# Kernel tuning notes

Measured on AMD Instinct MI355X. Metric: run time of the kernel, lower is better.

Reference implementation:

```python
import jax, jax.numpy as jnp
import numpy as np
import math

FMAPS = [(80, 0.06), (40, 0.12), (20, 0.24), (10, 0.48), (5, 0.72)]
SPLITS = [0, 6400, 8000, 8400, 8500, 8525]
N_LEVELS = 5
N_CAND = 9
ALPHA_REG = 1.0   # config.reg_weights
GAMMA, F_ALPHA = 2.0, 0.25


def _make_priors():
    ps = []
    for f, s in FMAPS:
        c = (np.arange(f, dtype=np.float32) + 0.5) / f
        cy, cx = np.meshgrid(c, c, indexing="ij")
        ps.append(np.stack([cx.ravel(), cy.ravel(),
                            np.full(f * f, s, np.float32),
                            np.full(f * f, s, np.float32)], 1))
    return jnp.asarray(np.concatenate(ps, 0))


def cxcy_to_xy(b):
    return jnp.concatenate([b[..., :2] - b[..., 2:] / 2, b[..., :2] + b[..., 2:] / 2], -1)


def xy_to_cxcy(b):
    return jnp.concatenate([(b[..., :2] + b[..., 2:]) / 2, b[..., 2:] - b[..., :2]], -1)


def gcxgcy_to_cxcy(g, priors):
    cxcy = g[..., :2] * priors[..., 2:] / 10.0 + priors[..., :2]
    wh = jnp.exp(g[..., 2:] / 5.0) * priors[..., 2:]
    return jnp.concatenate([cxcy, wh], -1)


def iou_matrix(a, b):  # a [K,4] corners, b [P,4] corners -> [K,P]
    lt = jnp.maximum(a[:, None, :2], b[None, :, :2])
    rb = jnp.minimum(a[:, None, 2:], b[None, :, 2:])
    wh = jnp.clip(rb - lt, 0.0)
    inter = wh[..., 0] * wh[..., 1]
    area_a = (a[:, 2] - a[:, 0]) * (a[:, 3] - a[:, 1])
    area_b = (b[:, 2] - b[:, 0]) * (b[:, 3] - b[:, 1])
    return inter / (area_a[:, None] + area_b[None, :] - inter)


def _assign_image(boxes_i, labels_i, locs_i, priors):
    # boxes_i [K,4] xyxy, labels_i [K] int, locs_i [P,4] encoded offsets
    gt_cxcy = xy_to_cxcy(boxes_i)
    per_level, pos_ov_all = [], []
    for l in range(N_LEVELS):
        pl = priors[SPLITS[l]:SPLITS[l + 1]]                       # [Pl,4] cxcywh
        dist = jnp.linalg.norm(gt_cxcy[:, None, :2] - pl[None, :, :2], axis=-1)  # [K,Pl]
        _, top_idx = jax.lax.top_k(-dist, N_CAND)                  # [K,9] closest priors
        ov = iou_matrix(boxes_i, cxcy_to_xy(pl))                   # [K,Pl]
        pos_ov = jnp.take_along_axis(ov, top_idx, axis=1)          # [K,9]
        pos_ov_all.append(pos_ov)
        per_level.append((pl, top_idx, pos_ov, locs_i[SPLITS[l]:SPLITS[l + 1]]))
    cat = jnp.concatenate(pos_ov_all, 1)                           # [K, 5*9]
    thr = cat.mean(1) + jnp.std(cat, axis=1, ddof=1)               # torch.std is unbiased

    labels_out, gt_match, dec_match, valid_all = [], [], [], []
    for l, (pl, top_idx, pos_ov, locs_l) in enumerate(per_level):
        cand = pl[top_idx]                                          # [K,9,4]
        inside = ((boxes_i[:, None, 0] < cand[..., 0]) & (cand[..., 0] < boxes_i[:, None, 2]) &
                  (boxes_i[:, None, 1] < cand[..., 1]) & (cand[..., 1] < boxes_i[:, None, 3]))
        cand_pos = (pos_ov > thr[:, None]) & inside                 # [K,9]
        masked = jnp.where(cand_pos, pos_ov, 0.0)                   # loop init current_max_iou=0
        best_ob = jnp.argmax(masked, axis=0)                        # [9], first-max == strict-> loop
        best_iou = jnp.max(masked, axis=0)
        valid = best_iou > 0.0                                      # [9]
        lab = jnp.where(valid, labels_i[best_ob], 0)
        Pl = SPLITS[l + 1] - SPLITS[l]
        # NB: original code indexes label array by candidate index c (bug kept faithfully)
        labels_out.append(jnp.zeros(Pl, jnp.int32).at[jnp.arange(N_CAND)].set(lab))
        decoded = cxcy_to_xy(gcxgcy_to_cxcy(locs_l, pl))            # [Pl,4]
        prior_idx = top_idx[best_ob, jnp.arange(N_CAND)]            # [9]
        dec_match.append(decoded[prior_idx])
        gt_match.append(boxes_i[best_ob])
        valid_all.append(valid)
    return (jnp.concatenate(labels_out),                            # [P]
            jnp.concatenate(gt_match, 0),                           # [45,4]
            jnp.concatenate(dec_match, 0),                          # [45,4]
            jnp.concatenate(valid_all))                             # [45]


def _ciou(pred, gt):  # corner boxes [N,4]
    w1, h1 = pred[:, 2] - pred[:, 0], pred[:, 3] - pred[:, 1]
    w2, h2 = gt[:, 2] - gt[:, 0], gt[:, 3] - gt[:, 1]
    lt = jnp.maximum(pred[:, :2], gt[:, :2]); rb = jnp.minimum(pred[:, 2:], gt[:, 2:])
    wh = jnp.clip(rb - lt, 0.0)
    inter = wh[:, 0] * wh[:, 1]
    union = w1 * h1 + w2 * h2 - inter
    iou = inter / union
    c1 = (pred[:, :2] + pred[:, 2:]) / 2; c2 = (gt[:, :2] + gt[:, 2:]) / 2
    rho2 = jnp.sum((c1 - c2) ** 2, -1)
    clt = jnp.minimum(pred[:, :2], gt[:, :2]); crb = jnp.maximum(pred[:, 2:], gt[:, 2:])
    cdiag = jnp.sum((crb - clt) ** 2, -1)
    v = (4.0 / math.pi ** 2) * (jnp.arctan(w2 / h2) - jnp.arctan(w1 / h1)) ** 2
    alpha = jax.lax.stop_gradient(v / (1.0 - iou + v))
    return jnp.clip(iou - rho2 / cdiag - alpha * v, -1.0, 1.0)


def _focal(logits, targets):  # logits [N,C], targets [N] in {0..C}, 0=background
    C = logits.shape[-1]
    cls = jnp.arange(1, C + 1)
    t = targets[:, None]
    p = jax.nn.sigmoid(logits)
    term1 = (1.0 - p) ** GAMMA * jax.nn.log_sigmoid(logits)
    term2 = p ** GAMMA * jax.nn.log_sigmoid(-logits)
    pos = (t == cls).astype(logits.dtype)
    neg = ((t != cls) & (t >= 0)).astype(logits.dtype)
    return -jnp.sum(pos * F_ALPHA * term1 + neg * (1.0 - F_ALPHA) * term2)


def setup_inputs():
    key = jax.random.key(0)
    k1, k2, k3, k4, k5 = jax.random.split(key, 5)
    B, K, C, P = 32, 16, 80, 8525
    lo = jax.random.uniform(k1, (B, K, 2), minval=0.05, maxval=0.55)
    sz = jax.random.uniform(k2, (B, K, 2), minval=0.08, maxval=0.35)
    boxes = jnp.concatenate([lo, lo + sz], -1)
    labels = jax.random.randint(k3, (B, K), 1, C + 1, dtype=jnp.int32)
    predicted_locs = jax.random.normal(k4, (B, P, 4), jnp.float32)
    predicted_scores = jax.random.normal(k5, (B, P, C), jnp.float32)
    return {"predicted_locs": predicted_locs, "predicted_scores": predicted_scores,
            "boxes": boxes, "labels": labels, "priors_cxcy": _make_priors()}


def reference(predicted_locs, predicted_scores, boxes, labels, priors_cxcy):
    tc, gt_m, dec_m, valid = jax.vmap(_assign_image, in_axes=(0, 0, 0, None))(
        boxes, labels, predicted_locs, priors_cxcy)
    tc_flat = tc.reshape(-1)
    n_pos = jnp.sum(tc_flat > 0).astype(jnp.float32)
    conf_loss = _focal(predicted_scores.reshape(-1, predicted_scores.shape[-1]), tc_flat) / n_pos
    ci = _ciou(dec_m.reshape(-1, 4), gt_m.reshape(-1, 4))
    vm = valid.reshape(-1).astype(jnp.float32)
    loc_loss = jnp.sum((1.0 - ci) * vm) / jnp.maximum(vm.sum(), 1.0)
    return conf_loss + ALPHA_REG * loc_loss
```

## Files before the change

kernel.cpp:

```cpp
#include <hip/hip_runtime.h>
#include <math.h>

#define KGT   16
#define NCAND 9
#define NLVL  5
#define NPRI  8525
#define NCLS  80
#define NIMG  32

#define SCAN_BLOCKS  10
#define FOCAL_BLOCKS 2038
#define TOTAL_BLOCKS 2048
#define NELEM (NIMG * NPRI * NCLS)
#define N4    (NELEM / 4)
#define NTASK (NIMG * KGT * NLVL)

#define OFF_IDXS  92160
#define OFF_PART  184320
#define OFF_IMG   192512

__device__ __forceinline__ float focal_elem(float x)
{
    float e  = __expf(-fabsf(x));
    float t  = 1.f + e;
    float r  = __builtin_amdgcn_rcpf(t);
    float sp = fmaxf(x, 0.f) + __logf(t);
    float nm = (x >= 0.f) ? 1.f : e;
    float p  = nm * r;
    return p * p * sp;
}

__device__ __forceinline__ float focal4(float4 v)
{
    return focal_elem(v.x) + focal_elem(v.y) + focal_elem(v.z) + focal_elem(v.w);
}

__global__ __launch_bounds__(256)
void atss_main(const float* __restrict__ scores,
               const float* __restrict__ boxes,
               const float* __restrict__ priors,
               float* __restrict__ povs,
               int*   __restrict__ idxs,
               float* __restrict__ partials)
{
    const int tid = threadIdx.x;
    const int blk = blockIdx.x;
    __shared__ float wsum[4];

    if (blk < SCAN_BLOCKS) {
        const int SPLc[5]  = {0, 6400, 8000, 8400, 8500};
        const int FDIM[5]  = {80, 40, 20, 10, 5};
        const int t = blk * 256 + tid;
        const int b = t / (KGT * NLVL);
        const int r = t % (KGT * NLVL);
        const int g = r / NLVL;
        const int l = r % NLVL;
        const int f    = FDIM[l];
        const int base = SPLc[l];

        float4 bx = ((const float4*)boxes)[b * KGT + g];
        const float gcx = (bx.x + bx.z) * 0.5f;
        const float gcy = (bx.y + bx.w) * 0.5f;

        const float ff = (float)f;
        int ix0 = (int)floorf(gcx * ff); ix0 = min(max(ix0, 0), f - 1);
        int iy0 = (int)floorf(gcy * ff); iy0 = min(max(iy0, 0), f - 1);
        int sx = min(max(ix0 - 2, 0), f - 5);
        int sy = min(max(iy0 - 2, 0), f - 5);

        unsigned long long L[NCAND];
        #pragma unroll
        for (int s = 0; s < NCAND; ++s) L[s] = ~0ull;

        for (int dy = 0; dy < 5; ++dy) {
            for (int dx = 0; dx < 5; ++dx) {
                int idx = (sy + dy) * f + (sx + dx);
                float2 pc = ((const float2*)priors)[(base + idx) * 2];
                float ddx = gcx - pc.x, ddy = gcy - pc.y;
                float dist = sqrtf(ddx * ddx + ddy * ddy);
                unsigned long long pk =
                    ((unsigned long long)__float_as_uint(dist) << 32) | (unsigned)idx;
                if (pk < L[NCAND - 1]) {
                    L[NCAND - 1] = pk;
                    #pragma unroll
                    for (int s = NCAND - 1; s >= 1; --s) {
                        if (L[s] < L[s - 1]) {
                            unsigned long long tw = L[s]; L[s] = L[s - 1]; L[s - 1] = tw;
                        } else break;
                    }
                }
            }
        }
        #pragma unroll
        for (int s = 0; s < NCAND; ++s) {
            int idx = (int)(unsigned)(L[s] & 0xffffffffull);
            float4 pr = ((const float4*)priors)[base + idx];
            float px0 = pr.x - pr.z * 0.5f, py0 = pr.y - pr.w * 0.5f;
            float px1 = pr.x + pr.z * 0.5f, py1 = pr.y + pr.w * 0.5f;
            float iw = fmaxf(fminf(bx.z, px1) - fmaxf(bx.x, px0), 0.f);
            float ih = fmaxf(fminf(bx.w, py1) - fmaxf(bx.y, py0), 0.f);
            float inter = iw * ih;
            float areaA = (bx.z - bx.x) * (bx.w - bx.y);
            float areaP = (px1 - px0) * (py1 - py0);
            povs[t * NCAND + s] = inter / (areaA + areaP - inter);
            idxs[t * NCAND + s] = idx;
        }
        return;
    }

    const float4* s4 = (const float4*)scores;
    const int S = FOCAL_BLOCKS * 256;
    int gid = (blk - SCAN_BLOCKS) * 256 + tid;
    float lsum = 0.f;
    for (int bse = gid; bse < N4; bse += 4 * S) {
        int i1 = bse + S, i2 = bse + 2 * S, i3 = bse + 3 * S;
        float4 v0 = s4[bse];
        float4 v1 = s4[min(i1, N4 - 1)];
        float4 v2 = s4[min(i2, N4 - 1)];
        float4 v3 = s4[min(i3, N4 - 1)];
        float t0 = focal4(v0);
        float t1 = focal4(v1);
        float t2 = focal4(v2);
        float t3 = focal4(v3);
        lsum += t0;
        lsum += (i1 < N4) ? t1 : 0.f;
        lsum += (i2 < N4) ? t2 : 0.f;
        lsum += (i3 < N4) ? t3 : 0.f;
    }
    #pragma unroll
    for (int off = 32; off > 0; off >>= 1) lsum += __shfl_down(lsum, off);
    if ((tid & 63) == 0) wsum[tid >> 6] = lsum;
    __syncthreads();
    if (tid == 0)
        partials[blk - SCAN_BLOCKS] = wsum[0] + wsum[1] + wsum[2] + wsum[3];
}

__global__ __launch_bounds__(256)
void atss_decide(const float* __restrict__ locs,
                 const float* __restrict__ scores,
                 const float* __restrict__ boxes,
                 const int*   __restrict__ labels,
                 const float* __restrict__ priors,
                 const float* __restrict__ povs,
                 const int*   __restrict__ idxs,
                 float* __restrict__ imgstats)
{
    const int tid = threadIdx.x;
    const int b = blockIdx.x;
    const int SPLc[6] = {0, 6400, 8000, 8400, 8500, 8525};

    __shared__ float pov[KGT * 45];
    __shared__ int   tix[KGT * 45];
    __shared__ float sbox[KGT][4];
    __shared__ int   slab[KGT];
    __shared__ float thr[KGT];
    __shared__ float rc, rl;
    __shared__ int   rn;

    if (tid == 0) { rc = 0.f; rl = 0.f; rn = 0; }
    for (int e = tid; e < KGT * 45; e += 256) {
        pov[e] = povs[b * (KGT * 45) + e];
        tix[e] = idxs[b * (KGT * 45) + e];
    }
    if (tid < KGT) {
        float4 bxv = ((const float4*)boxes)[b * KGT + tid];
        sbox[tid][0] = bxv.x; sbox[tid][1] = bxv.y;
        sbox[tid][2] = bxv.z; sbox[tid][3] = bxv.w;
        slab[tid] = labels[b * KGT + tid];
    }
    __syncthreads();

    if (tid < KGT) {
        float s = 0.f;
        for (int q = 0; q < 45; ++q) s += pov[tid * 45 + q];
        float mean = s / 45.f;
        float ss = 0.f;
        for (int q = 0; q < 45; ++q) { float d = pov[tid * 45 + q] - mean; ss += d * d; }
        thr[tid] = mean + sqrtf(ss / 44.f);
    }
    __syncthreads();

    if (tid < NLVL * NCAND) {
        int l = tid / NCAND, j = tid % NCAND;
        float bestv = -1.f; int bestg = 0;
        #pragma unroll
        for (int gg = 0; gg < KGT; ++gg) {
            float m = pov[gg * 45 + tid];
            int pi = tix[gg * 45 + tid];
            float4 pr = ((const float4*)priors)[SPLc[l] + pi];
            bool inside = (sbox[gg][0] < pr.x) && (pr.x < sbox[gg][2]) &&
                          (sbox[gg][1] < pr.y) && (pr.y < sbox[gg][3]);
            float mm = ((m > thr[gg]) && inside) ? m : 0.f;
            if (mm > bestv) { bestv = mm; bestg = gg; }
        }
        if (bestv > 0.f) {
            int lab = slab[bestg];
            long pos = (long)b * NPRI + SPLc[l] + j;
            float x  = scores[pos * NCLS + (lab - 1)];
            float e  = expf(-fabsf(x));
            float l1 = log1pf(e);
            float spp = fmaxf(x, 0.f) + l1;
            float spn = fmaxf(-x, 0.f) + l1;
            float p   = (x >= 0.f) ? 1.f / (1.f + e) : e / (1.f + e);
            float corr = 0.25f * (1.f - p) * (1.f - p) * spn - 0.75f * p * p * spp;

            int pi = tix[bestg * 45 + tid];
            float4 pr = ((const float4*)priors)[SPLc[l] + pi];
            float4 lc = ((const float4*)locs)[b * NPRI + SPLc[l] + pi];
            float cx = lc.x * pr.z / 10.f + pr.x;
            float cy = lc.y * pr.w / 10.f + pr.y;
            float w  = expf(lc.z / 5.f) * pr.z;
            float h  = expf(lc.w / 5.f) * pr.w;
            float qx0 = cx - w * 0.5f, qy0 = cy - h * 0.5f;
            float qx1 = cx + w * 0.5f, qy1 = cy + h * 0.5f;
            float gx0 = sbox[bestg][0], gy0 = sbox[bestg][1];
            float gx1 = sbox[bestg][2], gy1 = sbox[bestg][3];
            float w1 = qx1 - qx0, h1 = qy1 - qy0, w2 = gx1 - gx0, h2 = gy1 - gy0;
            float iw = fmaxf(fminf(qx1, gx1) - fmaxf(qx0, gx0), 0.f);
            float ih = fmaxf(fminf(qy1, gy1) - fmaxf(qy0, gy0), 0.f);
            float inter = iw * ih;
            float iou = inter / (w1 * h1 + w2 * h2 - inter);
            float dcx = (qx0 + qx1) * 0.5f - (gx0 + gx1) * 0.5f;
            float dcy = (qy0 + qy1) * 0.5f - (gy0 + gy1) * 0.5f;
            float rho2 = dcx * dcx + dcy * dcy;
            float ex = fmaxf(qx1, gx1) - fminf(qx0, gx0);
            float ey = fmaxf(qy1, gy1) - fminf(qy0, gy0);
            float cdiag = ex * ex + ey * ey;
            float da = atanf(w2 / h2) - atanf(w1 / h1);
            float v  = 0.4052847345693511f * da * da;
            float alpha = v / (1.f - iou + v);
            float ci = iou - rho2 / cdiag - alpha * v;
            ci = fminf(fmaxf(ci, -1.f), 1.f);

            atomicAdd(&rc, corr);
            atomicAdd(&rl, 1.f - ci);
            atomicAdd(&rn, 1);
        }
    }
    __syncthreads();
    if (tid == 0) {
        imgstats[b * 3 + 0] = rc;
        imgstats[b * 3 + 1] = rl;
        imgstats[b * 3 + 2] = (float)rn;
    }
}

__global__ __launch_bounds__(256)
void atss_finalize(const float* __restrict__ partials,
                   const float* __restrict__ imgstats,
                   float* __restrict__ out)
{
    const int tid = threadIdx.x;
    __shared__ float wsum[4];
    float lsum = 0.f;
    for (int i = tid; i < FOCAL_BLOCKS; i += 256) lsum += partials[i];
    #pragma unroll
    for (int off = 32; off > 0; off >>= 1) lsum += __shfl_down(lsum, off);
    if ((tid & 63) == 0) wsum[tid >> 6] = lsum;
    __syncthreads();
    if (tid == 0) {
        float base = 0.75f * (wsum[0] + wsum[1] + wsum[2] + wsum[3]);
        float corr = 0.f, loc = 0.f, cnt = 0.f;
        for (int b = 0; b < NIMG; ++b) {
            corr += imgstats[b * 3 + 0];
            loc  += imgstats[b * 3 + 1];
            cnt  += imgstats[b * 3 + 2];
        }
        float conf = (base + corr) / cnt;
        float locl = loc / fmaxf(cnt, 1.f);
        out[0] = conf + locl;
    }
}

extern "C" void kernel_launch(void* const* d_in, const int* in_sizes, int n_in,
                              void* d_out, int out_size, void* d_ws, size_t ws_size,
                              hipStream_t stream)
{
    const float* locs   = (const float*)d_in[0];
    const float* scores = (const float*)d_in[1];
    const float* boxes  = (const float*)d_in[2];
    const int*   labels = (const int*)d_in[3];
    const float* priors = (const float*)d_in[4];
    float* out = (float*)d_out;

    float* povs     = (float*)d_ws;
    int*   idxs     = (int*)((char*)d_ws + OFF_IDXS);
    float* partials = (float*)((char*)d_ws + OFF_PART);
    float* imgstats = (float*)((char*)d_ws + OFF_IMG);

    atss_main<<<TOTAL_BLOCKS, 256, 0, stream>>>(scores, boxes, priors,
                                                povs, idxs, partials);
    atss_decide<<<NIMG, 256, 0, stream>>>(locs, scores, boxes, labels, priors,
                                          povs, idxs, imgstats);
    atss_finalize<<<1, 256, 0, stream>>>(partials, imgstats, out);
}
```

Baseline: 154.8 us.

## Fuse candidate scan and per-image decision into main focal kernel

Merges the candidate-scan and per-image assignment kernels into the focal-loss kernel. 32 extra blocks each handle one image, keeping IoU candidates in shared memory instead of a global workspace round trip. The focal path now uses a fixed 3-stage software-prefetched unroll with 2016 blocks and launch bounds asking for 8 blocks per CU. This removes one kernel launch and the workspace traffic. The cost is heavier per-image blocks that may run at the tail, plus higher register pressure from the prefetch buffers.

```diff
diff --git a/kernel.cpp b/kernel.cpp
--- a/kernel.cpp
+++ b/kernel.cpp
@@ -8,16 +8,13 @@
 #define NCLS  80
 #define NIMG  32
 
-#define SCAN_BLOCKS  10
-#define FOCAL_BLOCKS 2038
-#define TOTAL_BLOCKS 2048
+#define FOCAL_BLOCKS 2016
+#define TOTAL_BLOCKS (FOCAL_BLOCKS + NIMG)
 #define NELEM (NIMG * NPRI * NCLS)
 #define N4    (NELEM / 4)
-#define NTASK (NIMG * KGT * NLVL)
-
-#define OFF_IDXS  92160
-#define OFF_PART  184320
-#define OFF_IMG   192512
+#define FS    (FOCAL_BLOCKS * 256)
+
+#define OFF_IMG 8192
 
 __device__ __forceinline__ float focal_elem(float x)
 {
@@ -35,32 +32,86 @@
     return focal_elem(v.x) + focal_elem(v.y) + focal_elem(v.z) + focal_elem(v.w);
 }
 
-__global__ __launch_bounds__(256)
-void atss_main(const float* __restrict__ scores,
+__global__ __launch_bounds__(256, 8)
+void atss_main(const float* __restrict__ locs,
+               const float* __restrict__ scores,
                const float* __restrict__ boxes,
+               const int*   __restrict__ labels,
                const float* __restrict__ priors,
-               float* __restrict__ povs,
-               int*   __restrict__ idxs,
-               float* __restrict__ partials)
+               float* __restrict__ partials,
+               float* __restrict__ imgstats)
 {
     const int tid = threadIdx.x;
     const int blk = blockIdx.x;
+
     __shared__ float wsum[4];
-
-    if (blk < SCAN_BLOCKS) {
-        const int SPLc[5]  = {0, 6400, 8000, 8400, 8500};
-        const int FDIM[5]  = {80, 40, 20, 10, 5};
-        const int t = blk * 256 + tid;
-        const int b = t / (KGT * NLVL);
-        const int r = t % (KGT * NLVL);
-        const int g = r / NLVL;
-        const int l = r % NLVL;
+    __shared__ float pov[KGT * 45];
+    __shared__ int   tix[KGT * 45];
+    __shared__ float sbox[KGT][4];
+    __shared__ int   slab[KGT];
+    __shared__ float thr[KGT];
+    __shared__ float rc, rl;
+    __shared__ int   rn;
+
+    if (blk < FOCAL_BLOCKS) {
+        const float4* s4 = (const float4*)scores;
+        const int gid = blk * 256 + tid;
+        const int kmax = (N4 - 1 - gid) / FS;
+        float lsum = 0.f;
+
+        float4 buf[4];
+        #pragma unroll
+        for (int u = 0; u < 4; ++u)
+            buf[u] = s4[min(gid + u * FS, N4 - 1)];
+
+        #pragma unroll
+        for (int g2 = 0; g2 < 3; ++g2) {
+            float4 nbuf[4];
+            if (g2 < 2) {
+                #pragma unroll
+                for (int u = 0; u < 4; ++u)
+                    nbuf[u] = s4[min(gid + ((g2 + 1) * 4 + u) * FS, N4 - 1)];
+            }
+            #pragma unroll
+            for (int u = 0; u < 4; ++u) {
+                float tv = focal4(buf[u]);
+                lsum += ((g2 * 4 + u) <= kmax) ? tv : 0.f;
+            }
+            if (g2 < 2) {
+                #pragma unroll
+                for (int u = 0; u < 4; ++u) buf[u] = nbuf[u];
+            }
+        }
+
+        #pragma unroll
+        for (int off = 32; off > 0; off >>= 1) lsum += __shfl_down(lsum, off);
+        if ((tid & 63) == 0) wsum[tid >> 6] = lsum;
+        __syncthreads();
+        if (tid == 0)
+            partials[blk] = wsum[0] + wsum[1] + wsum[2] + wsum[3];
+        return;
+    }
+
+    const int b = blk - FOCAL_BLOCKS;
+    const int SPLc[6] = {0, 6400, 8000, 8400, 8500, 8525};
+    const int FDIM[5] = {80, 40, 20, 10, 5};
+
+    if (tid == 0) { rc = 0.f; rl = 0.f; rn = 0; }
+    if (tid < KGT) {
+        float4 bxv = ((const float4*)boxes)[b * KGT + tid];
+        sbox[tid][0] = bxv.x; sbox[tid][1] = bxv.y;
+        sbox[tid][2] = bxv.z; sbox[tid][3] = bxv.w;
+        slab[tid] = labels[b * KGT + tid];
+    }
+    __syncthreads();
+
+    if (tid < KGT * NLVL) {
+        const int g = tid / NLVL;
+        const int l = tid % NLVL;
         const int f    = FDIM[l];
         const int base = SPLc[l];
-
-        float4 bx = ((const float4*)boxes)[b * KGT + g];
-        const float gcx = (bx.x + bx.z) * 0.5f;
-        const float gcy = (bx.y + bx.w) * 0.5f;
+        const float gcx = (sbox[g][0] + sbox[g][2]) * 0.5f;
+        const float gcy = (sbox[g][1] + sbox[g][3]) * 0.5f;
 
         const float ff = (float)f;
         int ix0 = (int)floorf(gcx * ff); ix0 = min(max(ix0, 0), f - 1);
@@ -97,76 +148,15 @@
             float4 pr = ((const float4*)priors)[base + idx];
             float px0 = pr.x - pr.z * 0.5f, py0 = pr.y - pr.w * 0.5f;
             float px1 = pr.x + pr.z * 0.5f, py1 = pr.y + pr.w * 0.5f;
-            float iw = fmaxf(fminf(bx.z, px1) - fmaxf(bx.x, px0), 0.f);
-            float ih = fmaxf(fminf(bx.w, py1) - fmaxf(bx.y, py0), 0.f);
+            float iw = fmaxf(fminf(sbox[g][2], px1) - fmaxf(sbox[g][0], px0), 0.f);
+            float ih = fmaxf(fminf(sbox[g][3], py1) - fmaxf(sbox[g][1], py0), 0.f);
             float inter = iw * ih;
-            float areaA = (bx.z - bx.x) * (bx.w - bx.y);
+            float areaA = (sbox[g][2] - sbox[g][0]) * (sbox[g][3] - sbox[g][1]);
             float areaP = (px1 - px0) * (py1 - py0);
-            povs[t * NCAND + s] = inter / (areaA + areaP - inter);
-            idxs[t * NCAND + s] = idx;
-        }
-        return;
-    }
-
-    const float4* s4 = (const float4*)scores;
-    const int S = FOCAL_BLOCKS * 256;
-    int gid = (blk - SCAN_BLOCKS) * 256 + tid;
-    float lsum = 0.f;
-    for (int bse = gid; bse < N4; bse += 4 * S) {
-        int i1 = bse + S, i2 = bse + 2 * S, i3 = bse + 3 * S;
-        float4 v0 = s4[bse];
-        float4 v1 = s4[min(i1, N4 - 1)];
-        float4 v2 = s4[min(i2, N4 - 1)];
-        float4 v3 = s4[min(i3, N4 - 1)];
-        float t0 = focal4(v0);
-        float t1 = focal4(v1);
-        float t2 = focal4(v2);
-        float t3 = focal4(v3);
-        lsum += t0;
-        lsum += (i1 < N4) ? t1 : 0.f;
-        lsum += (i2 < N4) ? t2 : 0.f;
-        lsum += (i3 < N4) ? t3 : 0.f;
-    }
-    #pragma unroll
-    for (int off = 32; off > 0; off >>= 1) lsum += __shfl_down(lsum, off);
-    if ((tid & 63) == 0) wsum[tid >> 6] = lsum;
-    __syncthreads();
-    if (tid == 0)
-        partials[blk - SCAN_BLOCKS] = wsum[0] + wsum[1] + wsum[2] + wsum[3];
-}
-
-__global__ __launch_bounds__(256)
-void atss_decide(const float* __restrict__ locs,
-                 const float* __restrict__ scores,
-                 const float* __restrict__ boxes,
-                 const int*   __restrict__ labels,
-                 const float* __restrict__ priors,
-                 const float* __restrict__ povs,
-                 const int*   __restrict__ idxs,
-                 float* __restrict__ imgstats)
-{
-    const int tid = threadIdx.x;
-    const int b = blockIdx.x;
-    const int SPLc[6] = {0, 6400, 8000, 8400, 8500, 8525};
-
-    __shared__ float pov[KGT * 45];
-    __shared__ int   tix[KGT * 45];
-    __shared__ float sbox[KGT][4];
-    __shared__ int   slab[KGT];
-    __shared__ float thr[KGT];
-    __shared__ float rc, rl;
-    __shared__ int   rn;
-
-    if (tid == 0) { rc = 0.f; rl = 0.f; rn = 0; }
-    for (int e = tid; e < KGT * 45; e += 256) {
-        pov[e] = povs[b * (KGT * 45) + e];
-        tix[e] = idxs[b * (KGT * 45) + e];
-    }
-    if (tid < KGT) {
-        float4 bxv = ((const float4*)boxes)[b * KGT + tid];
-        sbox[tid][0] = bxv.x; sbox[tid][1] = bxv.y;
-        sbox[tid][2] = bxv.z; sbox[tid][3] = bxv.w;
-        slab[tid] = labels[b * KGT + tid];
+            int o = g * 45 + l * NCAND + s;
+            pov[o] = inter / (areaA + areaP - inter);
+            tix[o] = idx;
+        }
     }
     __syncthreads();
 
@@ -283,14 +273,10 @@
     const float* priors = (const float*)d_in[4];
     float* out = (float*)d_out;
 
-    float* povs     = (float*)d_ws;
-    int*   idxs     = (int*)((char*)d_ws + OFF_IDXS);
-    float* partials = (float*)((char*)d_ws + OFF_PART);
+    float* partials = (float*)d_ws;
     float* imgstats = (float*)((char*)d_ws + OFF_IMG);
 
-    atss_main<<<TOTAL_BLOCKS, 256, 0, stream>>>(scores, boxes, priors,
-                                                povs, idxs, partials);
-    atss_decide<<<NIMG, 256, 0, stream>>>(locs, scores, boxes, labels, priors,
-                                          povs, idxs, imgstats);
+    atss_main<<<TOTAL_BLOCKS, 256, 0, stream>>>(locs, scores, boxes, labels,
+                                                priors, partials, imgstats);
     atss_finalize<<<1, 256, 0, stream>>>(partials, imgstats, out);
 }
```

Measured after the change: 156.0 us. Within noise of the previous version (+0.8%).
